# Kernel optimization log

Hardware: AMD Instinct MI355X
Metric: run time of the kernel (lower is better)

The kernel has to match this reference:

```python
import jax, jax.numpy as jnp
import numpy as np

EPS = 1e-12  # F.normalize default eps

def setup_inputs() -> dict:
    key = jax.random.key(0)
    k1, k2, k3, k4, k5, k6 = jax.random.split(key, 6)
    N, F, T = 2000, 64, 24
    x = jax.random.normal(k1, (N, F, T), dtype=jnp.float32)
    adj_norm = jax.random.uniform(k2, (N, N), dtype=jnp.float32)
    weight = jax.random.normal(k3, (N, F, F), dtype=jnp.float32) / (F * F)
    Wq = jax.random.normal(k4, (F, F), dtype=jnp.float32) * 0.1
    Wk = jax.random.normal(k5, (F, F), dtype=jnp.float32) * 0.1
    Wv = jax.random.normal(k6, (F, F), dtype=jnp.float32) * 0.1
    return {"x": x, "adj_norm": adj_norm, "weight": weight, "Wq": Wq, "Wk": Wk, "Wv": Wv}

def reference(x, adj_norm, weight, Wq, Wk, Wv):
    # x: (N, F, T)
    N, F, T = x.shape
    # ---- Spatial_Attention_layer ----
    z = jnp.transpose(x, (2, 0, 1))                     # (T, N, F)
    nrm = jnp.sqrt(jnp.sum(z * z, axis=2, keepdims=True))
    z1 = z / jnp.maximum(nrm, EPS)
    score = jnp.einsum('tnf,tmf->tnm', z1, z1)          # (T, N, N)
    score = jax.nn.softmax(score, axis=-1)
    adj = adj_norm[None, :, :] * score                  # (T, N, N)
    # ---- CrossAttention fusion (shape-preserving self-attn over T) ----
    xt = jnp.transpose(x, (0, 2, 1))                    # (N, T, F)
    q = xt @ Wq
    k = xt @ Wk
    v = xt @ Wv
    a = jax.nn.softmax(jnp.einsum('ntf,nsf->nts', q, k) / jnp.sqrt(jnp.float32(F)), axis=-1)
    xf = jnp.einsum('nts,nsf->ntf', a, v)               # (N, T, F)
    xp = jnp.transpose(xf, (1, 0, 2))                   # (T, N, F) == x.permute(2,0,1)
    # ---- einsum('phh,bhi->bhi', adj, x): multiply by sum_p diag(adj[p]) ----
    diag_adj = jnp.sum(jnp.diagonal(adj, axis1=1, axis2=2), axis=0)      # (N,)
    # ---- einsum('bhi,pii->bhi', y, weight): multiply by sum_p diag(weight[p]) ----
    diag_w = jnp.sum(jnp.diagonal(weight, axis1=1, axis2=2), axis=0)     # (F,)
    out = xp * diag_adj[None, :, None] * diag_w[None, None, :]           # (T, N, F)
    return jnp.transpose(out, (1, 2, 0))                # (N, F, T)
```

## Files before the change

### kernel.cpp

```cpp
#include <hip/hip_runtime.h>
#include <hip/hip_bf16.h>

#define N_   2000
#define NP   2048
#define F_   64
#define T_   24

typedef short  v8s  __attribute__((ext_vector_type(8)));
typedef float  v4f  __attribute__((ext_vector_type(4)));
typedef unsigned short v4us __attribute__((ext_vector_type(4)));

__device__ __forceinline__ unsigned short f2bf(float f) {
  unsigned int u = __float_as_uint(f);
  u += 0x7fffu + ((u >> 16) & 1u);
  return (unsigned short)(u >> 16);
}

__global__ __launch_bounds__(256) void fill_z(const float* __restrict__ x,
                                              unsigned short* __restrict__ zb) {
  int n = blockIdx.x;
  int tid = threadIdx.x, wave = tid >> 6, lane = tid & 63;
  if (n >= N_) {
    for (int t = wave; t < T_; t += 4) zb[(t * NP + n) * F_ + lane] = 0;
    return;
  }
  __shared__ float xs[F_ * 25];
  const float* xn = x + n * (F_ * T_);
  for (int i = tid; i < F_ * T_; i += 256)
    xs[(i / T_) * 25 + (i % T_)] = xn[i];
  __syncthreads();
  for (int t = wave; t < T_; t += 4) {
    float v = xs[lane * 25 + t];
    float ss = v * v;
    #pragma unroll
    for (int m = 1; m < 64; m <<= 1) ss += __shfl_xor(ss, m);
    float nrm = fmaxf(sqrtf(ss), 1e-12f);
    zb[(t * NP + n) * F_ + lane] = f2bf(v / nrm);
  }
}

__global__ __launch_bounds__(256) void prep_wT(const float* __restrict__ wq,
                                               const float* __restrict__ wk,
                                               const float* __restrict__ wv,
                                               unsigned short* __restrict__ wT) {
  const float* src = (blockIdx.x == 0) ? wq : (blockIdx.x == 1) ? wk : wv;
  unsigned short* dst = wT + blockIdx.x * 4096;
  for (int i = threadIdx.x; i < 4096; i += 256) {
    int fi = i >> 6, fo = i & 63;
    dst[fo * 64 + fi] = f2bf(src[i]);
  }
}

__global__ __launch_bounds__(256) void diag_w_k(const float* __restrict__ w,
                                                float* __restrict__ dw) {
  int f = blockIdx.x, tid = threadIdx.x;
  float s = 0.f;
  for (int p = tid; p < N_; p += 256) s += w[p * (F_ * F_) + f * (F_ + 1)];
  #pragma unroll
  for (int m = 1; m < 64; m <<= 1) s += __shfl_xor(s, m);
  __shared__ float red[4];
  if ((tid & 63) == 0) red[tid >> 6] = s;
  __syncthreads();
  if (tid == 0) dw[f] = red[0] + red[1] + red[2] + red[3];
}

__global__ __launch_bounds__(256) void gram_expsum(const unsigned short* __restrict__ zb,
                                                   float* __restrict__ rowsum) {
  int rb = blockIdx.x, cb = blockIdx.y, t = blockIdx.z;
  int wave = threadIdx.x >> 6, lane = threadIdx.x & 63;
  int lr = lane & 15, lk = (lane >> 4) * 8;
  const unsigned short* z = zb + t * (NP * F_);
  int r0 = rb * 256 + wave * 64;

  v8s a[4][2];
  #pragma unroll
  for (int rg = 0; rg < 4; rg++)
    #pragma unroll
    for (int kb = 0; kb < 2; kb++)
      a[rg][kb] = *(const v8s*)(z + (r0 + rg * 16 + lr) * F_ + kb * 32 + lk);

  float acc[16];
  #pragma unroll
  for (int i = 0; i < 16; i++) acc[i] = 0.f;

  int c0 = cb * 512, c1 = (cb == 3) ? N_ : c0 + 512;
  const unsigned short* bp = z + (c0 + lr) * F_ + lk;
  v4f cz = {0.f, 0.f, 0.f, 0.f};

  for (int c = c0; c < c1; c += 16) {
    v8s b0 = *(const v8s*)(bp);
    v8s b1 = *(const v8s*)(bp + 32);
    bp += 16 * F_;
    #pragma unroll
    for (int rg = 0; rg < 4; rg++) {
      v4f C = __builtin_amdgcn_mfma_f32_16x16x32_bf16(a[rg][0], b0, cz, 0, 0, 0);
      C = __builtin_amdgcn_mfma_f32_16x16x32_bf16(a[rg][1], b1, C, 0, 0, 0);
      #pragma unroll
      for (int i = 0; i < 4; i++) acc[rg * 4 + i] += __expf(C[i] - 1.0f);
    }
  }
  #pragma unroll
  for (int i = 0; i < 16; i++) {
    acc[i] += __shfl_xor(acc[i], 1);
    acc[i] += __shfl_xor(acc[i], 2);
    acc[i] += __shfl_xor(acc[i], 4);
    acc[i] += __shfl_xor(acc[i], 8);
  }
  if (lr == 0) {
    float* rs = rowsum + t * NP;
    #pragma unroll
    for (int rg = 0; rg < 4; rg++)
      #pragma unroll
      for (int i = 0; i < 4; i++) {
        int r = r0 + rg * 16 + (lane >> 4) * 4 + i;
        if (r < N_) atomicAdd(&rs[r], acc[rg * 4 + i]);
      }
  }
}

__global__ __launch_bounds__(256) void diag_adj_k(const float* __restrict__ adj,
                                                  const float* __restrict__ rowsum,
                                                  float* __restrict__ da) {
  int n = blockIdx.x * 256 + threadIdx.x;
  if (n >= N_) return;
  float s = 0.f;
  #pragma unroll
  for (int t = 0; t < T_; t++) s += 1.0f / rowsum[t * NP + n];
  da[n] = adj[n * (N_ + 1)] * s;
}

__global__ __launch_bounds__(256) void cross_attn(const float* __restrict__ x,
                                                  const unsigned short* __restrict__ wT,
                                                  const float* __restrict__ dadj_g,
                                                  const float* __restrict__ dw_g,
                                                  float* __restrict__ out) {
  __shared__ __align__(16) unsigned short lds[4 * 8192];
  int wave = threadIdx.x >> 6, lane = threadIdx.x & 63;
  int n = blockIdx.x * 4 + wave;
  unsigned short* xt = lds + wave * 8192;
  unsigned short* q  = xt + 2048;
  unsigned short* k  = xt + 4096;
  unsigned short* vT = xt + 6144;
  unsigned short* p  = xt;
  int lr = lane & 15, lk = (lane >> 4) * 8;
  int row0q = (lane >> 4) * 4;
  v4f cz = {0.f, 0.f, 0.f, 0.f};

  const float* xn = x + n * (F_ * T_);
  #pragma unroll
  for (int j = 0; j < 24; j++) {
    int i = j * 64 + lane;
    float v = xn[i];
    xt[(i % T_) * 64 + (i / T_)] = f2bf(v);
  }
  { v8s z8 = {0,0,0,0,0,0,0,0}; *(v8s*)(xt + 24 * 64 + lane * 8) = z8; }

  v8s xa[2][2];
  #pragma unroll
  for (int rt = 0; rt < 2; rt++)
    #pragma unroll
    for (int kb = 0; kb < 2; kb++)
      xa[rt][kb] = *(const v8s*)(xt + (rt * 16 + lr) * 64 + kb * 32 + lk);

  #pragma unroll
  for (int m = 0; m < 3; m++) {
    const unsigned short* wt = wT + m * 4096;
    unsigned short* dst = (m == 0) ? q : k;
    #pragma unroll
    for (int ct = 0; ct < 4; ct++) {
      v8s b0 = *(const v8s*)(wt + (ct * 16 + lr) * 64 + lk);
      v8s b1 = *(const v8s*)(wt + (ct * 16 + lr) * 64 + 32 + lk);
      int col = ct * 16 + lr;
      #pragma unroll
      for (int rt = 0; rt < 2; rt++) {
        v4f C = __builtin_amdgcn_mfma_f32_16x16x32_bf16(xa[rt][0], b0, cz, 0, 0, 0);
        C = __builtin_amdgcn_mfma_f32_16x16x32_bf16(xa[rt][1], b1, C, 0, 0, 0);
        int r0 = rt * 16 + row0q;
        if (m < 2) {
          #pragma unroll
          for (int i = 0; i < 4; i++) dst[(r0 + i) * 64 + col] = f2bf(C[i]);
        } else {
          v4us pk = { f2bf(C[0]), f2bf(C[1]), f2bf(C[2]), f2bf(C[3]) };
          *(v4us*)(vT + col * 32 + r0) = pk;
        }
      }
    }
  }

  v8s qa[2][2];
  #pragma unroll
  for (int rt = 0; rt < 2; rt++)
    #pragma unroll
    for (int kb = 0; kb < 2; kb++)
      qa[rt][kb] = *(const v8s*)(q + (rt * 16 + lr) * 64 + kb * 32 + lk);

  float ev[2][2][4];
  #pragma unroll
  for (int ct = 0; ct < 2; ct++) {
    v8s b0 = *(const v8s*)(k + (ct * 16 + lr) * 64 + lk);
    v8s b1 = *(const v8s*)(k + (ct * 16 + lr) * 64 + 32 + lk);
    int col = ct * 16 + lr;
    #pragma unroll
    for (int rt = 0; rt < 2; rt++) {
      v4f C = __builtin_amdgcn_mfma_f32_16x16x32_bf16(qa[rt][0], b0, cz, 0, 0, 0);
      C = __builtin_amdgcn_mfma_f32_16x16x32_bf16(qa[rt][1], b1, C, 0, 0, 0);
      #pragma unroll
      for (int i = 0; i < 4; i++)
        ev[ct][rt][i] = (col < T_) ? __expf(C[i] * 0.125f) : 0.0f;
    }
  }
  #pragma unroll
  for (int rt = 0; rt < 2; rt++)
    #pragma unroll
    for (int i = 0; i < 4; i++) {
      float r = ev[0][rt][i] + ev[1][rt][i];
      r += __shfl_xor(r, 1); r += __shfl_xor(r, 2);
      r += __shfl_xor(r, 4); r += __shfl_xor(r, 8);
      float inv = 1.0f / r;
      int row = rt * 16 + row0q + i;
      p[row * 32 + lr]      = f2bf(ev[0][rt][i] * inv);
      p[row * 32 + 16 + lr] = f2bf(ev[1][rt][i] * inv);
    }

  v8s pa[2];
  #pragma unroll
  for (int rt = 0; rt < 2; rt++)
    pa[rt] = *(const v8s*)(p + (rt * 16 + lr) * 32 + lk);
  float dadj = dadj_g[n];
  float* outn = out + n * (F_ * T_);
  #pragma unroll
  for (int ct = 0; ct < 4; ct++) {
    v8s vb = *(const v8s*)(vT + (ct * 16 + lr) * 32 + lk);
    float sc = dadj * dw_g[ct * 16 + lr];
    #pragma unroll
    for (int rt = 0; rt < 2; rt++) {
      v4f C = __builtin_amdgcn_mfma_f32_16x16x32_bf16(pa[rt], vb, cz, 0, 0, 0);
      int r0 = rt * 16 + row0q;
      if (r0 < T_) {
        v4f o;
        #pragma unroll
        for (int i = 0; i < 4; i++) o[i] = C[i] * sc;
        *(v4f*)(outn + (ct * 16 + lr) * T_ + r0) = o;
      }
    }
  }
}

extern "C" void kernel_launch(void* const* d_in, const int* in_sizes, int n_in,
                              void* d_out, int out_size, void* d_ws, size_t ws_size,
                              hipStream_t stream) {
  const float* x   = (const float*)d_in[0];
  const float* adj = (const float*)d_in[1];
  const float* w   = (const float*)d_in[2];
  const float* wq  = (const float*)d_in[3];
  const float* wk  = (const float*)d_in[4];
  const float* wv  = (const float*)d_in[5];
  float* out = (float*)d_out;

  char* ws = (char*)d_ws;
  unsigned short* zb     = (unsigned short*)ws;
  float*          rowsum = (float*)(ws + 6291456);
  float*          dadj   = (float*)(ws + 6291456 + 196608);
  float*          dw     = (float*)(ws + 6291456 + 196608 + 8192);
  unsigned short* wT     = (unsigned short*)(ws + 6291456 + 196608 + 8192 + 256);

  hipMemsetAsync(rowsum, 0, T_ * NP * sizeof(float), stream);
  hipLaunchKernelGGL(fill_z,      dim3(NP),       dim3(256), 0, stream, x, zb);
  hipLaunchKernelGGL(prep_wT,     dim3(3),        dim3(256), 0, stream, wq, wk, wv, wT);
  hipLaunchKernelGGL(diag_w_k,    dim3(F_),       dim3(256), 0, stream, w, dw);
  hipLaunchKernelGGL(gram_expsum, dim3(8, 4, 24), dim3(256), 0, stream, zb, rowsum);
  hipLaunchKernelGGL(diag_adj_k,  dim3(8),        dim3(256), 0, stream, adj, rowsum, dadj);
  hipLaunchKernelGGL(cross_attn,  dim3(500),      dim3(256), 0, stream, x, wT, dadj, dw, out);
}
```

Measured before the change: 167.9 us.

## Merge prep kernels and replace rowsum atomics with per-block partials

```diff
diff --git a/kernel.cpp b/kernel.cpp
--- a/kernel.cpp
+++ b/kernel.cpp
@@ -16,56 +16,58 @@
   return (unsigned short)(u >> 16);
 }
 
-__global__ __launch_bounds__(256) void fill_z(const float* __restrict__ x,
-                                              unsigned short* __restrict__ zb) {
-  int n = blockIdx.x;
+__global__ __launch_bounds__(256) void prep(const float* __restrict__ x,
+                                            const float* __restrict__ w,
+                                            const float* __restrict__ wq,
+                                            const float* __restrict__ wk,
+                                            const float* __restrict__ wv,
+                                            unsigned short* __restrict__ zb,
+                                            float* __restrict__ dw,
+                                            unsigned short* __restrict__ wT) {
+  __shared__ float xs[F_ * 25];
+  __shared__ float red[4];
+  int b = blockIdx.x;
   int tid = threadIdx.x, wave = tid >> 6, lane = tid & 63;
-  if (n >= N_) {
-    for (int t = wave; t < T_; t += 4) zb[(t * NP + n) * F_ + lane] = 0;
-    return;
-  }
-  __shared__ float xs[F_ * 25];
-  const float* xn = x + n * (F_ * T_);
-  for (int i = tid; i < F_ * T_; i += 256)
-    xs[(i / T_) * 25 + (i % T_)] = xn[i];
-  __syncthreads();
-  for (int t = wave; t < T_; t += 4) {
-    float v = xs[lane * 25 + t];
-    float ss = v * v;
-    #pragma unroll
-    for (int m = 1; m < 64; m <<= 1) ss += __shfl_xor(ss, m);
-    float nrm = fmaxf(sqrtf(ss), 1e-12f);
-    zb[(t * NP + n) * F_ + lane] = f2bf(v / nrm);
-  }
-}
-
-__global__ __launch_bounds__(256) void prep_wT(const float* __restrict__ wq,
-                                               const float* __restrict__ wk,
-                                               const float* __restrict__ wv,
-                                               unsigned short* __restrict__ wT) {
-  const float* src = (blockIdx.x == 0) ? wq : (blockIdx.x == 1) ? wk : wv;
-  unsigned short* dst = wT + blockIdx.x * 4096;
-  for (int i = threadIdx.x; i < 4096; i += 256) {
-    int fi = i >> 6, fo = i & 63;
-    dst[fo * 64 + fi] = f2bf(src[i]);
-  }
-}
-
-__global__ __launch_bounds__(256) void diag_w_k(const float* __restrict__ w,
-                                                float* __restrict__ dw) {
-  int f = blockIdx.x, tid = threadIdx.x;
-  float s = 0.f;
-  for (int p = tid; p < N_; p += 256) s += w[p * (F_ * F_) + f * (F_ + 1)];
-  #pragma unroll
-  for (int m = 1; m < 64; m <<= 1) s += __shfl_xor(s, m);
-  __shared__ float red[4];
-  if ((tid & 63) == 0) red[tid >> 6] = s;
-  __syncthreads();
-  if (tid == 0) dw[f] = red[0] + red[1] + red[2] + red[3];
+
+  if (b < NP) {
+    int n = b;
+    if (n >= N_) {
+      for (int t = wave; t < T_; t += 4) zb[(t * NP + n) * F_ + lane] = 0;
+      return;
+    }
+    const float* xn = x + n * (F_ * T_);
+    for (int i = tid; i < F_ * T_; i += 256)
+      xs[(i / T_) * 25 + (i % T_)] = xn[i];
+    __syncthreads();
+    for (int t = wave; t < T_; t += 4) {
+      float v = xs[lane * 25 + t];
+      float ss = v * v;
+      #pragma unroll
+      for (int m = 1; m < 64; m <<= 1) ss += __shfl_xor(ss, m);
+      float nrm = fmaxf(sqrtf(ss), 1e-12f);
+      zb[(t * NP + n) * F_ + lane] = f2bf(v / nrm);
+    }
+  } else if (b < NP + 64) {
+    int f = b - NP;
+    float s = 0.f;
+    for (int p = tid; p < N_; p += 256) s += w[p * (F_ * F_) + f * (F_ + 1)];
+    #pragma unroll
+    for (int m = 1; m < 64; m <<= 1) s += __shfl_xor(s, m);
+    if (lane == 0) red[wave] = s;
+    __syncthreads();
+    if (tid == 0) dw[f] = red[0] + red[1] + red[2] + red[3];
+  } else {
+    for (int i = tid; i < 3 * 4096; i += 256) {
+      int m = i >> 12, r = i & 4095;
+      const float* src = (m == 0) ? wq : (m == 1) ? wk : wv;
+      int fi = r >> 6, fo = r & 63;
+      wT[m * 4096 + fo * 64 + fi] = f2bf(src[r]);
+    }
+  }
 }
 
 __global__ __launch_bounds__(256) void gram_expsum(const unsigned short* __restrict__ zb,
-                                                   float* __restrict__ rowsum) {
+                                                   float* __restrict__ partial) {
   int rb = blockIdx.x, cb = blockIdx.y, t = blockIdx.z;
   int wave = threadIdx.x >> 6, lane = threadIdx.x & 63;
   int lr = lane & 15, lk = (lane >> 4) * 8;
@@ -86,6 +88,7 @@
   int c0 = cb * 512, c1 = (cb == 3) ? N_ : c0 + 512;
   const unsigned short* bp = z + (c0 + lr) * F_ + lk;
   v4f cz = {0.f, 0.f, 0.f, 0.f};
+  const float INV_E = 0.36787944117144233f;
 
   for (int c = c0; c < c1; c += 16) {
     v8s b0 = *(const v8s*)(bp);
@@ -96,7 +99,8 @@
       v4f C = __builtin_amdgcn_mfma_f32_16x16x32_bf16(a[rg][0], b0, cz, 0, 0, 0);
       C = __builtin_amdgcn_mfma_f32_16x16x32_bf16(a[rg][1], b1, C, 0, 0, 0);
       #pragma unroll
-      for (int i = 0; i < 4; i++) acc[rg * 4 + i] += __expf(C[i] - 1.0f);
+      for (int i = 0; i < 4; i++)
+        acc[rg * 4 + i] = fmaf(__expf(C[i]), INV_E, acc[rg * 4 + i]);
     }
   }
   #pragma unroll
@@ -107,31 +111,19 @@
     acc[i] += __shfl_xor(acc[i], 8);
   }
   if (lr == 0) {
-    float* rs = rowsum + t * NP;
+    float* ps = partial + (cb * T_ + t) * NP;
     #pragma unroll
     for (int rg = 0; rg < 4; rg++)
       #pragma unroll
-      for (int i = 0; i < 4; i++) {
-        int r = r0 + rg * 16 + (lane >> 4) * 4 + i;
-        if (r < N_) atomicAdd(&rs[r], acc[rg * 4 + i]);
-      }
-  }
-}
-
-__global__ __launch_bounds__(256) void diag_adj_k(const float* __restrict__ adj,
-                                                  const float* __restrict__ rowsum,
-                                                  float* __restrict__ da) {
-  int n = blockIdx.x * 256 + threadIdx.x;
-  if (n >= N_) return;
-  float s = 0.f;
-  #pragma unroll
-  for (int t = 0; t < T_; t++) s += 1.0f / rowsum[t * NP + n];
-  da[n] = adj[n * (N_ + 1)] * s;
+      for (int i = 0; i < 4; i++)
+        ps[r0 + rg * 16 + (lane >> 4) * 4 + i] = acc[rg * 4 + i];
+  }
 }
 
 __global__ __launch_bounds__(256) void cross_attn(const float* __restrict__ x,
                                                   const unsigned short* __restrict__ wT,
-                                                  const float* __restrict__ dadj_g,
+                                                  const float* __restrict__ adj,
+                                                  const float* __restrict__ partial,
                                                   const float* __restrict__ dw_g,
                                                   float* __restrict__ out) {
   __shared__ __align__(16) unsigned short lds[4 * 8192];
@@ -146,6 +138,17 @@
   int row0q = (lane >> 4) * 4;
   v4f cz = {0.f, 0.f, 0.f, 0.f};
 
+  float invsum = 0.f;
+  if (lane < T_) {
+    float s = 0.f;
+    #pragma unroll
+    for (int cb = 0; cb < 4; cb++) s += partial[(cb * T_ + lane) * NP + n];
+    invsum = 1.0f / s;
+  }
+  #pragma unroll
+  for (int m = 1; m < 64; m <<= 1) invsum += __shfl_xor(invsum, m);
+  float dadj = adj[n * (N_ + 1)] * invsum;
+
   const float* xn = x + n * (F_ * T_);
   #pragma unroll
   for (int j = 0; j < 24; j++) {
@@ -226,7 +229,6 @@
   #pragma unroll
   for (int rt = 0; rt < 2; rt++)
     pa[rt] = *(const v8s*)(p + (rt * 16 + lr) * 32 + lk);
-  float dadj = dadj_g[n];
   float* outn = out + n * (F_ * T_);
   #pragma unroll
   for (int ct = 0; ct < 4; ct++) {
@@ -258,17 +260,14 @@
   float* out = (float*)d_out;
 
   char* ws = (char*)d_ws;
-  unsigned short* zb     = (unsigned short*)ws;
-  float*          rowsum = (float*)(ws + 6291456);
-  float*          dadj   = (float*)(ws + 6291456 + 196608);
-  float*          dw     = (float*)(ws + 6291456 + 196608 + 8192);
-  unsigned short* wT     = (unsigned short*)(ws + 6291456 + 196608 + 8192 + 256);
-
-  hipMemsetAsync(rowsum, 0, T_ * NP * sizeof(float), stream);
-  hipLaunchKernelGGL(fill_z,      dim3(NP),       dim3(256), 0, stream, x, zb);
-  hipLaunchKernelGGL(prep_wT,     dim3(3),        dim3(256), 0, stream, wq, wk, wv, wT);
-  hipLaunchKernelGGL(diag_w_k,    dim3(F_),       dim3(256), 0, stream, w, dw);
-  hipLaunchKernelGGL(gram_expsum, dim3(8, 4, 24), dim3(256), 0, stream, zb, rowsum);
-  hipLaunchKernelGGL(diag_adj_k,  dim3(8),        dim3(256), 0, stream, adj, rowsum, dadj);
-  hipLaunchKernelGGL(cross_attn,  dim3(500),      dim3(256), 0, stream, x, wT, dadj, dw, out);
-}
+  unsigned short* zb      = (unsigned short*)ws;
+  float*          partial = (float*)(ws + 6291456);
+  float*          dw      = (float*)(ws + 6291456 + 786432);
+  unsigned short* wT      = (unsigned short*)(ws + 6291456 + 786432 + 256);
+
+  hipLaunchKernelGGL(prep,        dim3(NP + 64 + 1), dim3(256), 0, stream,
+                     x, w, wq, wk, wv, zb, dw, wT);
+  hipLaunchKernelGGL(gram_expsum, dim3(8, 4, 24),    dim3(256), 0, stream, zb, partial);
+  hipLaunchKernelGGL(cross_attn,  dim3(500),         dim3(256), 0, stream,
+                     x, wT, adj, partial, dw, out);
+}
```

Result: faster. 153.9 us (-8.3%).
